# Optimization experiments

Measured on AMD Instinct MI355X. Metric: run time of the kernel, lower is better.

The kernel has to match this reference:

```python
import jax, jax.numpy as jnp
import numpy as np

EMBED_DIM = 1024
NUM_HEADS = 16
HEAD_DIM = EMBED_DIM // NUM_HEADS


def setup_inputs() -> dict:
    key = jax.random.key(0)
    ks = jax.random.split(key, 12)
    B, Nq, Nkv, D = 4, 1024, 1024, EMBED_DIM
    s = 1.0 / np.sqrt(D)
    return {
        "query": jax.random.normal(ks[0], (B, Nq, D), jnp.float32),
        "key_value": jax.random.normal(ks[1], (B, Nkv, D), jnp.float32),
        "Wq": jax.random.normal(ks[2], (D, D), jnp.float32) * s,
        "bq": jnp.zeros((D,), jnp.float32),
        "Wk": jax.random.normal(ks[3], (D, D), jnp.float32) * s,
        "bk": jnp.zeros((D,), jnp.float32),
        "Wv": jax.random.normal(ks[4], (D, D), jnp.float32) * s,
        "bv": jnp.zeros((D,), jnp.float32),
        "Wo": jax.random.normal(ks[5], (D, D), jnp.float32) * s,
        "bo": jnp.zeros((D,), jnp.float32),
        "gamma": jnp.ones((D,), jnp.float32),
        "beta": jnp.zeros((D,), jnp.float32),
    }


def reference(query, key_value, Wq, bq, Wk, bk, Wv, bv, Wo, bo, gamma, beta):
    B, Nq, D = query.shape
    Nkv = key_value.shape[1]
    H, Hd = NUM_HEADS, HEAD_DIM
    # projections -> [B, H, N, Hd]
    q = (query @ Wq + bq).reshape(B, Nq, H, Hd).transpose(0, 2, 1, 3)
    k = (key_value @ Wk + bk).reshape(B, Nkv, H, Hd).transpose(0, 2, 1, 3)
    v = (key_value @ Wv + bv).reshape(B, Nkv, H, Hd).transpose(0, 2, 1, 3)
    scores = jnp.einsum("bhqd,bhkd->bhqk", q, k) / jnp.sqrt(jnp.float32(Hd))
    attn = jax.nn.softmax(scores, axis=-1)  # dropout = identity at eval
    out = jnp.einsum("bhqk,bhkd->bhqd", attn, v)
    out = out.transpose(0, 2, 1, 3).reshape(B, Nq, D)
    out = out @ Wo + bo
    # residual + LayerNorm (eps = 1e-5, torch default)
    x = query + out
    mu = jnp.mean(x, axis=-1, keepdims=True)
    var = jnp.mean(jnp.square(x - mu), axis=-1, keepdims=True)
    return (x - mu) / jnp.sqrt(var + 1e-5) * gamma + beta
```

## Files before the change

kernel.cpp:

```cpp
#include <hip/hip_runtime.h>

typedef unsigned short u16;
typedef unsigned int u32;
typedef __attribute__((ext_vector_type(4))) unsigned short u16x4;
typedef __attribute__((ext_vector_type(8))) short short8;
typedef __attribute__((ext_vector_type(4))) float f32x4;

#define MFMA16(a, b, c) __builtin_amdgcn_mfma_f32_16x16x32_bf16(a, b, c, 0, 0, 0)

__device__ __forceinline__ u16 f2bf(float f) {
  unsigned u = __builtin_bit_cast(unsigned, f);
  u += 0x7fffu + ((u >> 16) & 1u);
  return (u16)(u >> 16);
}

__device__ __forceinline__ u32 cvtpk(float lo, float hi) {
  u32 r;
  asm("v_cvt_pk_bf16_f32 %0, %1, %2" : "=v"(r) : "v"(lo), "v"(hi));
  return r;
}

__device__ __forceinline__ void gl_lds16(const void* g, void* l) {
  __builtin_amdgcn_global_load_lds((const __attribute__((address_space(1))) char*)g,
                                   (__attribute__((address_space(3))) char*)l, 16, 0, 0);
}

__global__ __launch_bounds__(256) void cvt_bf16_k(const float* __restrict__ in,
                                                  u16* __restrict__ out) {
  int i = blockIdx.x * 256 + threadIdx.x;
  float4 v = ((const float4*)in)[i];
  u16x4 o;
  o.x = f2bf(v.x); o.y = f2bf(v.y); o.z = f2bf(v.z); o.w = f2bf(v.w);
  ((u16x4*)out)[i] = o;
}

__global__ __launch_bounds__(256) void wt_k(const float* __restrict__ W0, const float* __restrict__ W1,
                                            const float* __restrict__ W2, const float* __restrict__ W3,
                                            u16* __restrict__ T0, u16* __restrict__ T1,
                                            u16* __restrict__ T2, u16* __restrict__ T3) {
  const float* W; u16* T;
  switch (blockIdx.z) {
    case 0: W = W0; T = T0; break;
    case 1: W = W1; T = T1; break;
    case 2: W = W2; T = T2; break;
    default: W = W3; T = T3; break;
  }
  __shared__ __align__(16) u16 t[64][72];
  const int k0 = blockIdx.y * 64, n0 = blockIdx.x * 64;
  const int tid = threadIdx.x;
  const int r = tid >> 4, c4 = (tid & 15) * 4;
#pragma unroll
  for (int i = 0; i < 4; i++) {
    float4 v = *(const float4*)(W + (k0 + r + i * 16) * 1024 + n0 + c4);
    u16x4 o;
    o.x = f2bf(v.x); o.y = f2bf(v.y); o.z = f2bf(v.z); o.w = f2bf(v.w);
    *(u16x4*)&t[r + i * 16][c4] = o;
  }
  __syncthreads();
#pragma unroll
  for (int i = 0; i < 4; i++) {
    int nr = r + i * 16;
    u16x4 o;
    o.x = t[c4 + 0][nr]; o.y = t[c4 + 1][nr]; o.z = t[c4 + 2][nr]; o.w = t[c4 + 3][nr];
    *(u16x4*)(T + (n0 + nr) * 1024 + k0 + c4) = o;
  }
}

__global__ __launch_bounds__(256, 3) void gemmqkv_k(
    const u16* __restrict__ qbf, const u16* __restrict__ kvbf,
    const u16* __restrict__ Wqt, const u16* __restrict__ Wkt, const u16* __restrict__ Wvt,
    const float* __restrict__ pbq, const float* __restrict__ pbk, const float* __restrict__ pbv,
    u16* __restrict__ Qh, u16* __restrict__ Kh, u16* __restrict__ Vth) {
  const int lin = blockIdx.x;
  const int swz = (lin & 7) * 96 + (lin >> 3);
  const int x = swz & 7, y = (swz >> 3) & 31, z = swz >> 8;

  const u16* A  = (z == 0) ? qbf : kvbf;
  const u16* Bt = (z == 0) ? Wqt : (z == 1 ? Wkt : Wvt);
  const float* bias = (z == 0) ? pbq : (z == 1 ? pbk : pbv);

  __shared__ __align__(16) u16 As[128 * 32];
  __shared__ __align__(16) u16 Bs[128 * 32];
  const int tid = threadIdx.x;
  const int l = tid & 63, w = tid >> 6;
  const int lr = l >> 4, lc = l & 15;
  const int wr = w >> 1, wc = w & 1;
  const int m0 = y * 128, n0 = x * 128;

  f32x4 acc[4][4] = {};

  const int sr = tid >> 2, sc = (tid & 3) * 8;
  const u16* Ag = A + (m0 + sr) * 1024 + sc;
  const u16* Bg = Bt + (n0 + sr) * 1024 + sc;
  u16* AsW = As + tid * 8;
  u16* BsW = Bs + tid * 8;

  for (int k0 = 0; k0 < 1024; k0 += 32) {
    __syncthreads();
    gl_lds16(Ag + k0, AsW);
    gl_lds16(Ag + 64 * 1024 + k0, AsW + 2048);
    gl_lds16(Bg + k0, BsW);
    gl_lds16(Bg + 64 * 1024 + k0, BsW + 2048);
    __syncthreads();
    const u16* PA = (z == 2) ? Bs : As;
    const u16* PB = (z == 2) ? As : Bs;
    short8 af[4], bf[4];
    const int ks8 = lr * 8;
#pragma unroll
    for (int m = 0; m < 4; m++)
      af[m] = *(const short8*)(PA + (wr * 64 + m * 16 + lc) * 32 + ks8);
#pragma unroll
    for (int n = 0; n < 4; n++)
      bf[n] = *(const short8*)(PB + (wc * 64 + n * 16 + lc) * 32 + ks8);
#pragma unroll
    for (int m = 0; m < 4; m++)
#pragma unroll
      for (int n = 0; n < 4; n++)
        acc[m][n] = MFMA16(af[m], bf[n], acc[m][n]);
  }

  if (z == 2) {
#pragma unroll
    for (int m = 0; m < 4; m++) {
#pragma unroll
      for (int r = 0; r < 4; r++) {
        int ncol = n0 + wr * 64 + m * 16 + lr * 4 + r;
        float bb = bias[ncol];
        int h = ncol >> 6, d = ncol & 63;
#pragma unroll
        for (int n = 0; n < 4; n++) {
          int tok = m0 + wc * 64 + n * 16 + lc;
          Vth[(((tok >> 10) * 16 + h) * 64 + d) * 1024 + (tok & 1023)] =
              f2bf(acc[m][n][r] + bb);
        }
      }
    }
  } else {
    u16* outb = (z == 0) ? Qh : Kh;
    const float scale = (z == 0) ? 0.125f : 1.0f;
#pragma unroll
    for (int m = 0; m < 4; m++)
#pragma unroll
      for (int n = 0; n < 4; n++) {
        int ncol = n0 + wc * 64 + n * 16 + lc;
        float bb = bias[ncol];
        int h = ncol >> 6, d = ncol & 63;
#pragma unroll
        for (int r = 0; r < 4; r++) {
          int tok = m0 + wr * 64 + m * 16 + lr * 4 + r;
          outb[(((tok >> 10) * 16 + h) * 1024 + (tok & 1023)) * 64 + d] =
              f2bf((acc[m][n][r] + bb) * scale);
        }
      }
  }
}

__global__ __launch_bounds__(256, 4) void gemmo_k(const u16* __restrict__ A,
                                                  const u16* __restrict__ Bt,
                                                  const float* __restrict__ bias,
                                                  float* __restrict__ outf) {
  const int lin = blockIdx.x;
  const int swz = (lin & 7) * 64 + (lin >> 3);
  const int x = swz & 15, y = swz >> 4;

  __shared__ __align__(16) u16 As[128 * 32];
  __shared__ __align__(16) u16 Bs[64 * 32];
  const int tid = threadIdx.x;
  const int l = tid & 63, w = tid >> 6;
  const int lr = l >> 4, lc = l & 15;
  const int wr = w >> 1, wc = w & 1;
  const int m0 = y * 128, n0 = x * 64;

  f32x4 acc[4][2] = {};
  const int sc = (tid & 3) * 8;
  const u16* Ag = A + (m0 + (tid >> 2)) * 1024 + sc;
  const u16* Bg = Bt + (n0 + (tid >> 2)) * 1024 + sc;

  for (int k0 = 0; k0 < 1024; k0 += 32) {
    __syncthreads();
    gl_lds16(Ag + k0, As + tid * 8);
    gl_lds16(Ag + 64 * 1024 + k0, As + 2048 + tid * 8);
    gl_lds16(Bg + k0, Bs + tid * 8);
    __syncthreads();
    short8 af[4], bf[2];
    const int ks8 = lr * 8;
#pragma unroll
    for (int m = 0; m < 4; m++)
      af[m] = *(const short8*)(As + (wr * 64 + m * 16 + lc) * 32 + ks8);
#pragma unroll
    for (int n = 0; n < 2; n++)
      bf[n] = *(const short8*)(Bs + (wc * 32 + n * 16 + lc) * 32 + ks8);
#pragma unroll
    for (int m = 0; m < 4; m++)
#pragma unroll
      for (int n = 0; n < 2; n++)
        acc[m][n] = MFMA16(af[m], bf[n], acc[m][n]);
  }
#pragma unroll
  for (int m = 0; m < 4; m++)
#pragma unroll
    for (int n = 0; n < 2; n++) {
      int ncol = n0 + wc * 32 + n * 16 + lc;
      float bb = bias[ncol];
#pragma unroll
      for (int r = 0; r < 4; r++) {
        int tok = m0 + wr * 64 + m * 16 + lr * 4 + r;
        outf[tok * 1024 + ncol] = acc[m][n][r] + bb;
      }
    }
}

__global__ __launch_bounds__(256, 4) void attn_k(const u16* __restrict__ Q,
                                                 const u16* __restrict__ K,
                                                 const u16* __restrict__ Vt,
                                                 u16* __restrict__ O) {
  const int bid = blockIdx.x;
  const int xcd = bid & 7, j = bid >> 3;
  const int bh = xcd + 8 * (j & 7);
  const int q0 = (j >> 3) * 64;
  const int tid = threadIdx.x;
  const int w = tid >> 6, l = tid & 63;
  const int lr = l >> 4, lc = l & 15;
  const u16* Qh = Q + bh * (1024 * 64);
  const u16* Kh = K + bh * (1024 * 64);
  const u16* Vh = Vt + bh * (64 * 1024);

  __shared__ __align__(16) u16 Ks[64 * 64];
  __shared__ __align__(16) u16 Vs[64 * 64];
  __shared__ __align__(16) u32 Plds[4][16][36];

  const int st_row = tid >> 3;
  const int st_cb = (tid & 7) * 16;
  const int sw1 = (st_cb ^ ((st_row & 7) << 4)) >> 1;
  const int st_row2 = st_row + 32;
  const int sw2 = (st_cb ^ ((st_row2 & 7) << 4)) >> 1;

  short8 bq[2];
#pragma unroll
  for (int ks = 0; ks < 2; ks++)
    bq[ks] = *(const short8*)(Qh + (q0 + w * 16 + lc) * 64 + ks * 32 + lr * 8);

  f32x4 oacc[4] = {};
  float mrun = -1e30f, lrun = 0.f;

  for (int kv0 = 0; kv0 < 1024; kv0 += 64) {
    __syncthreads();
    gl_lds16(Kh + (kv0 + st_row) * 64 + sw1, Ks + tid * 8);
    gl_lds16(Kh + (kv0 + st_row2) * 64 + sw2, Ks + 2048 + tid * 8);
    gl_lds16(Vh + st_row * 1024 + kv0 + sw1, Vs + tid * 8);
    gl_lds16(Vh + st_row2 * 1024 + kv0 + sw2, Vs + 2048 + tid * 8);
    __syncthreads();

    f32x4 s[4] = {};
#pragma unroll
    for (int mk = 0; mk < 4; mk++) {
      const int krow = mk * 16 + lc;
      const u16* kp = Ks + krow * 64;
#pragma unroll
      for (int ks = 0; ks < 2; ks++) {
        const int cb = (ks * 64 + lr * 16) ^ ((krow & 7) << 4);
        short8 ak = *(const short8*)(kp + (cb >> 1));
        s[mk] = MFMA16(ak, bq[ks], s[mk]);
      }
    }

    float mx = s[0][0];
#pragma unroll
    for (int mk = 0; mk < 4; mk++)
#pragma unroll
      for (int r = 0; r < 4; r++) mx = fmaxf(mx, s[mk][r]);
    mx = fmaxf(mx, __shfl_xor(mx, 16));
    mx = fmaxf(mx, __shfl_xor(mx, 32));
    float mnew = fmaxf(mrun, mx);
    float alpha = __expf(mrun - mnew);
    mrun = mnew;
    float ps = 0.f;
#pragma unroll
    for (int mk = 0; mk < 4; mk++)
#pragma unroll
      for (int r = 0; r < 4; r++) {
        float p = __expf(s[mk][r] - mnew);
        s[mk][r] = p;
        ps += p;
      }
    ps += __shfl_xor(ps, 16);
    ps += __shfl_xor(ps, 32);
    lrun = lrun * alpha + ps;

    u32* PW = &Plds[w][lc][0];
#pragma unroll
    for (int mk = 0; mk < 4; mk++)
#pragma unroll
      for (int rr = 0; rr < 2; rr++)
        PW[mk * 8 + lr * 2 + rr] = cvtpk(s[mk][2 * rr], s[mk][2 * rr + 1]);

    float alr[4];
#pragma unroll
    for (int r = 0; r < 4; r++) alr[r] = __shfl(alpha, lr * 4 + r);
#pragma unroll
    for (int nd = 0; nd < 4; nd++)
#pragma unroll
      for (int r = 0; r < 4; r++) oacc[nd][r] *= alr[r];

#pragma unroll
    for (int ks = 0; ks < 2; ks++) {
      short8 ap = *(const short8*)&Plds[w][lc][ks * 16 + lr * 4];
#pragma unroll
      for (int nd = 0; nd < 4; nd++) {
        const int vrow = nd * 16 + lc;
        const int cb = (ks * 64 + lr * 16) ^ ((vrow & 7) << 4);
        short8 bv = *(const short8*)(Vs + vrow * 64 + (cb >> 1));
        oacc[nd] = MFMA16(ap, bv, oacc[nd]);
      }
    }
  }

  float inv = 1.f / lrun;
  float invr[4];
#pragma unroll
  for (int r = 0; r < 4; r++) invr[r] = __shfl(inv, lr * 4 + r);
  const int b = bh >> 4, h = bh & 15;
#pragma unroll
  for (int r = 0; r < 4; r++) {
    int row = b * 1024 + q0 + w * 16 + lr * 4 + r;
#pragma unroll
    for (int nd = 0; nd < 4; nd++)
      O[row * 1024 + h * 64 + nd * 16 + lc] = f2bf(oacc[nd][r] * invr[r]);
  }
}

__global__ __launch_bounds__(256) void ln_k(const float* __restrict__ q,
                                            const float* __restrict__ p2,
                                            const float* __restrict__ gamma,
                                            const float* __restrict__ beta,
                                            float* __restrict__ out) {
  const int row = blockIdx.x, tid = threadIdx.x;
  float4 xq = ((const float4*)(q + row * 1024))[tid];
  float4 xp = ((const float4*)(p2 + row * 1024))[tid];
  float4 x = {xq.x + xp.x, xq.y + xp.y, xq.z + xp.z, xq.w + xp.w};
  float s = x.x + x.y + x.z + x.w;
#pragma unroll
  for (int off = 1; off < 64; off <<= 1) s += __shfl_xor(s, off);
  __shared__ float red[8];
  const int w = tid >> 6;
  if ((tid & 63) == 0) red[w] = s;
  __syncthreads();
  float mu = (red[0] + red[1] + red[2] + red[3]) * (1.0f / 1024.0f);
  float4 dx = {x.x - mu, x.y - mu, x.z - mu, x.w - mu};
  float s2 = dx.x * dx.x + dx.y * dx.y + dx.z * dx.z + dx.w * dx.w;
#pragma unroll
  for (int off = 1; off < 64; off <<= 1) s2 += __shfl_xor(s2, off);
  if ((tid & 63) == 0) red[4 + w] = s2;
  __syncthreads();
  float var = (red[4] + red[5] + red[6] + red[7]) * (1.0f / 1024.0f);
  float rs = rsqrtf(var + 1e-5f);
  float4 g = ((const float4*)gamma)[tid];
  float4 bb = ((const float4*)beta)[tid];
  float4 o = {dx.x * rs * g.x + bb.x, dx.y * rs * g.y + bb.y,
              dx.z * rs * g.z + bb.z, dx.w * rs * g.w + bb.w};
  ((float4*)(out + row * 1024))[tid] = o;
}

extern "C" void kernel_launch(void* const* d_in, const int* in_sizes, int n_in,
                              void* d_out, int out_size, void* d_ws, size_t ws_size,
                              hipStream_t stream) {
  const float* query = (const float*)d_in[0];
  const float* kv    = (const float*)d_in[1];
  const float* Wq = (const float*)d_in[2];
  const float* bq = (const float*)d_in[3];
  const float* Wk = (const float*)d_in[4];
  const float* bk = (const float*)d_in[5];
  const float* Wv = (const float*)d_in[6];
  const float* bv = (const float*)d_in[7];
  const float* Wo = (const float*)d_in[8];
  const float* bo = (const float*)d_in[9];
  const float* gamma = (const float*)d_in[10];
  const float* beta  = (const float*)d_in[11];
  float* out = (float*)d_out;

  char* ws = (char*)d_ws;
  const size_t MB = 1u << 20;
  u16* qbf  = (u16*)(ws + 0 * MB);
  u16* kvbf = (u16*)(ws + 8 * MB);
  u16* Wqt  = (u16*)(ws + 16 * MB);
  u16* Wkt  = (u16*)(ws + 18 * MB);
  u16* Wvt  = (u16*)(ws + 20 * MB);
  u16* Wot  = (u16*)(ws + 22 * MB);
  u16* Qh   = (u16*)(ws + 24 * MB);
  u16* Kh   = (u16*)(ws + 32 * MB);
  u16* Vth  = (u16*)(ws + 40 * MB);
  u16* attO = (u16*)(ws + 48 * MB);
  float* p2 = (float*)(ws + 56 * MB);

  cvt_bf16_k<<<dim3(4096), dim3(256), 0, stream>>>(query, qbf);
  cvt_bf16_k<<<dim3(4096), dim3(256), 0, stream>>>(kv, kvbf);
  wt_k<<<dim3(16, 16, 4), dim3(256), 0, stream>>>(Wq, Wk, Wv, Wo, Wqt, Wkt, Wvt, Wot);

  gemmqkv_k<<<dim3(768), dim3(256), 0, stream>>>(qbf, kvbf, Wqt, Wkt, Wvt,
                                                 bq, bk, bv, Qh, Kh, Vth);

  attn_k<<<dim3(1024), dim3(256), 0, stream>>>(Qh, Kh, Vth, attO);

  gemmo_k<<<dim3(512), dim3(256), 0, stream>>>(attO, Wot, bo, p2);

  ln_k<<<dim3(4096), dim3(256), 0, stream>>>(query, p2, gamma, beta, out);
}
```

Baseline: 116.9 us.

## Double-buffer K/V tiles in attention, use exp2 with lazy rescaling

The attention kernel now double-buffers K and V tiles in LDS, prefetching the next tile with async global-to-LDS loads while the current one is computed, gated by explicit vmcnt waits and barriers. The softmax switches to native exp2, with log2(e) folded into the Q scale. The running-max rescale of the accumulator is skipped unless the max grows by more than a threshold. MFMA sections get raised wave priority, and launch bounds drop occupancy to 3 to make room for the doubled LDS. The aim is to hide load latency and cut transcendental and rescale work, at the cost of lower occupancy and more LDS.

```diff
diff --git a/kernel.cpp b/kernel.cpp
--- a/kernel.cpp
+++ b/kernel.cpp
@@ -17,6 +17,12 @@
 __device__ __forceinline__ u32 cvtpk(float lo, float hi) {
   u32 r;
   asm("v_cvt_pk_bf16_f32 %0, %1, %2" : "=v"(r) : "v"(lo), "v"(hi));
+  return r;
+}
+
+__device__ __forceinline__ float ex2(float x) {
+  float r;
+  asm("v_exp_f32 %0, %1" : "=v"(r) : "v"(x));
   return r;
 }
 
@@ -137,7 +143,7 @@
     }
   } else {
     u16* outb = (z == 0) ? Qh : Kh;
-    const float scale = (z == 0) ? 0.125f : 1.0f;
+    const float scale = (z == 0) ? 0.18033688f : 1.0f;
 #pragma unroll
     for (int m = 0; m < 4; m++)
 #pragma unroll
@@ -210,7 +216,7 @@
     }
 }
 
-__global__ __launch_bounds__(256, 4) void attn_k(const u16* __restrict__ Q,
+__global__ __launch_bounds__(256, 3) void attn_k(const u16* __restrict__ Q,
                                                  const u16* __restrict__ K,
                                                  const u16* __restrict__ Vt,
                                                  u16* __restrict__ O) {
@@ -225,8 +231,8 @@
   const u16* Kh = K + bh * (1024 * 64);
   const u16* Vh = Vt + bh * (64 * 1024);
 
-  __shared__ __align__(16) u16 Ks[64 * 64];
-  __shared__ __align__(16) u16 Vs[64 * 64];
+  __shared__ __align__(16) u16 Ks[2][64 * 64];
+  __shared__ __align__(16) u16 Vs[2][64 * 64];
   __shared__ __align__(16) u32 Plds[4][16][36];
 
   const int st_row = tid >> 3;
@@ -243,19 +249,35 @@
   f32x4 oacc[4] = {};
   float mrun = -1e30f, lrun = 0.f;
 
-  for (int kv0 = 0; kv0 < 1024; kv0 += 64) {
-    __syncthreads();
-    gl_lds16(Kh + (kv0 + st_row) * 64 + sw1, Ks + tid * 8);
-    gl_lds16(Kh + (kv0 + st_row2) * 64 + sw2, Ks + 2048 + tid * 8);
-    gl_lds16(Vh + st_row * 1024 + kv0 + sw1, Vs + tid * 8);
-    gl_lds16(Vh + st_row2 * 1024 + kv0 + sw2, Vs + 2048 + tid * 8);
-    __syncthreads();
+  gl_lds16(Kh + st_row * 64 + sw1, &Ks[0][tid * 8]);
+  gl_lds16(Kh + st_row2 * 64 + sw2, &Ks[0][2048 + tid * 8]);
+  gl_lds16(Vh + st_row * 1024 + sw1, &Vs[0][tid * 8]);
+  gl_lds16(Vh + st_row2 * 1024 + sw2, &Vs[0][2048 + tid * 8]);
+
+  for (int t = 0; t < 16; ++t) {
+    const int pb = t & 1;
+    if (t < 15) {
+      const int kvn = (t + 1) * 64;
+      gl_lds16(Kh + (kvn + st_row) * 64 + sw1, &Ks[pb ^ 1][tid * 8]);
+      gl_lds16(Kh + (kvn + st_row2) * 64 + sw2, &Ks[pb ^ 1][2048 + tid * 8]);
+      gl_lds16(Vh + st_row * 1024 + kvn + sw1, &Vs[pb ^ 1][tid * 8]);
+      gl_lds16(Vh + st_row2 * 1024 + kvn + sw2, &Vs[pb ^ 1][2048 + tid * 8]);
+      asm volatile("s_waitcnt vmcnt(4)" ::: "memory");
+    } else {
+      asm volatile("s_waitcnt vmcnt(0)" ::: "memory");
+    }
+    __builtin_amdgcn_s_barrier();
+    asm volatile("" ::: "memory");
+
+    const u16* Kb = Ks[pb];
+    const u16* Vb = Vs[pb];
 
     f32x4 s[4] = {};
+    __builtin_amdgcn_s_setprio(1);
 #pragma unroll
     for (int mk = 0; mk < 4; mk++) {
       const int krow = mk * 16 + lc;
-      const u16* kp = Ks + krow * 64;
+      const u16* kp = Kb + krow * 64;
 #pragma unroll
       for (int ks = 0; ks < 2; ks++) {
         const int cb = (ks * 64 + lr * 16) ^ ((krow & 7) << 4);
@@ -263,29 +285,48 @@
         s[mk] = MFMA16(ak, bq[ks], s[mk]);
       }
     }
-
-    float mx = s[0][0];
-#pragma unroll
-    for (int mk = 0; mk < 4; mk++)
-#pragma unroll
-      for (int r = 0; r < 4; r++) mx = fmaxf(mx, s[mk][r]);
+    __builtin_amdgcn_s_setprio(0);
+
+    float mx;
+    {
+      float a = fmaxf(fmaxf(s[0][0], s[0][1]), fmaxf(s[0][2], s[0][3]));
+      float b = fmaxf(fmaxf(s[1][0], s[1][1]), fmaxf(s[1][2], s[1][3]));
+      float c = fmaxf(fmaxf(s[2][0], s[2][1]), fmaxf(s[2][2], s[2][3]));
+      float d = fmaxf(fmaxf(s[3][0], s[3][1]), fmaxf(s[3][2], s[3][3]));
+      mx = fmaxf(fmaxf(a, b), fmaxf(c, d));
+    }
     mx = fmaxf(mx, __shfl_xor(mx, 16));
     mx = fmaxf(mx, __shfl_xor(mx, 32));
-    float mnew = fmaxf(mrun, mx);
-    float alpha = __expf(mrun - mnew);
-    mrun = mnew;
-    float ps = 0.f;
+
+    if (!__all(mx <= mrun + 8.f)) {
+      float mnew = fmaxf(mrun, mx);
+      float alpha = ex2(mrun - mnew);
+      mrun = mnew;
+      lrun *= alpha;
+      float alr[4];
+#pragma unroll
+      for (int r = 0; r < 4; r++) alr[r] = __shfl(alpha, lr * 4 + r);
+#pragma unroll
+      for (int nd = 0; nd < 4; nd++)
+#pragma unroll
+        for (int r = 0; r < 4; r++) oacc[nd][r] *= alr[r];
+    }
+
 #pragma unroll
     for (int mk = 0; mk < 4; mk++)
 #pragma unroll
-      for (int r = 0; r < 4; r++) {
-        float p = __expf(s[mk][r] - mnew);
-        s[mk][r] = p;
-        ps += p;
-      }
+      for (int r = 0; r < 4; r++) s[mk][r] = ex2(s[mk][r] - mrun);
+    float ps;
+    {
+      float a = (s[0][0] + s[0][1]) + (s[0][2] + s[0][3]);
+      float b = (s[1][0] + s[1][1]) + (s[1][2] + s[1][3]);
+      float c = (s[2][0] + s[2][1]) + (s[2][2] + s[2][3]);
+      float d = (s[3][0] + s[3][1]) + (s[3][2] + s[3][3]);
+      ps = (a + b) + (c + d);
+    }
     ps += __shfl_xor(ps, 16);
     ps += __shfl_xor(ps, 32);
-    lrun = lrun * alpha + ps;
+    lrun += ps;
 
     u32* PW = &Plds[w][lc][0];
 #pragma unroll
@@ -294,14 +335,7 @@
       for (int rr = 0; rr < 2; rr++)
         PW[mk * 8 + lr * 2 + rr] = cvtpk(s[mk][2 * rr], s[mk][2 * rr + 1]);
 
-    float alr[4];
-#pragma unroll
-    for (int r = 0; r < 4; r++) alr[r] = __shfl(alpha, lr * 4 + r);
-#pragma unroll
-    for (int nd = 0; nd < 4; nd++)
-#pragma unroll
-      for (int r = 0; r < 4; r++) oacc[nd][r] *= alr[r];
-
+    __builtin_amdgcn_s_setprio(1);
 #pragma unroll
     for (int ks = 0; ks < 2; ks++) {
       short8 ap = *(const short8*)&Plds[w][lc][ks * 16 + lr * 4];
@@ -309,10 +343,14 @@
       for (int nd = 0; nd < 4; nd++) {
         const int vrow = nd * 16 + lc;
         const int cb = (ks * 64 + lr * 16) ^ ((vrow & 7) << 4);
-        short8 bv = *(const short8*)(Vs + vrow * 64 + (cb >> 1));
+        short8 bv = *(const short8*)(Vb + vrow * 64 + (cb >> 1));
         oacc[nd] = MFMA16(ap, bv, oacc[nd]);
       }
     }
+    __builtin_amdgcn_s_setprio(0);
+
+    asm volatile("" ::: "memory");
+    __builtin_amdgcn_s_barrier();
   }
 
   float inv = 1.f / lrun;
```

Measured after the change: 123.1 us. 5.3% more time.
